# Performance work log

Measured on AMD Instinct MI355X. Metric: run time of the kernel, lower is better.

## Reference

```python
import jax, jax.numpy as jnp
import numpy as np
from jax import lax

T, B, I, H = 512, 256, 128, 256

def setup_inputs() -> dict:
    key = jax.random.key(0)
    k1, k2, k3, k4 = jax.random.split(key, 4)
    x = jax.random.normal(k1, (T, B, I), dtype=jnp.float32)
    h0 = jnp.zeros((B, H), dtype=jnp.float32)
    Wi = jax.random.normal(k2, (H, I), dtype=jnp.float32) * (1.0 / np.sqrt(I))
    Wh = jax.random.normal(k3, (H, H), dtype=jnp.float32) * (1.0 / np.sqrt(H))
    bh = jax.random.normal(k4, (H,), dtype=jnp.float32) * 0.01
    return {"x": x, "h0": h0, "Wi": Wi, "Wh": Wh, "bh": bh}

def reference(x, h0, Wi, Wh, bh):
    # Precompute input projection for all timesteps: [T, B, H]
    xi = jnp.einsum("tbi,hi->tbh", x, Wi) + bh
    def step(h, xi_t):
        h_new = jnp.tanh(xi_t + h @ Wh.T)
        return h_new, h_new
    _, hs = lax.scan(step, h0, xi)
    return hs  # [T, B, H] hidden states, matching torch stack(out[1:])
```

## Files before the change

### kernel.cpp

```cpp
#include <hip/hip_runtime.h>
#include <hip/hip_bf16.h>
#include <math.h>

#define TT 512
#define BB 256
#define II 128
#define HH 256

#define TANH_S 2.885390043258667f


#define FCHUNK(CNT, A0,A1,B0,B1,C0,C1,D0,D1, H0,H1) \
        "s_waitcnt lgkmcnt(" CNT ")\n" \
        "v_pk_fma_f32 v[32:33], v[" A0 "], v[" H0 "], v[32:33]\n" \
        "v_pk_fma_f32 v[34:35], v[" B0 "], v[" H0 "], v[34:35]\n" \
        "v_pk_fma_f32 v[36:37], v[" C0 "], v[" H0 "], v[36:37]\n" \
        "v_pk_fma_f32 v[38:39], v[" D0 "], v[" H0 "], v[38:39]\n" \
        "v_pk_fma_f32 v[32:33], v[" A1 "], v[" H1 "], v[32:33]\n" \
        "v_pk_fma_f32 v[34:35], v[" B1 "], v[" H1 "], v[34:35]\n" \
        "v_pk_fma_f32 v[36:37], v[" C1 "], v[" H1 "], v[36:37]\n" \
        "v_pk_fma_f32 v[38:39], v[" D1 "], v[" H1 "], v[38:39]\n"

#define SCALE_PAIR(P) "v_pk_mul_f32 v[" P "], v[" P "], v[26:27]\n"

__global__ __launch_bounds__(512, 2) void rnn_fused_kernel(
    const float* __restrict__ x,  const float* __restrict__ h0,
    const float* __restrict__ Wi, const float* __restrict__ Wh,
    const float* __restrict__ bh, float* __restrict__ out)
{
    __shared__ float hbuf[928];

    const int tid  = threadIdx.x;
    const int b    = blockIdx.x;
    const int lane = tid & 63;
    const int q    = tid >> 6;
    const int kg   = (lane & 3) | ((lane >> 1) & 4);
    const int cg   = ((lane >> 2) & 1) | ((lane >> 3) & 6);
    const int col0 = 32 * q + 4 * cg;
    const int col  = col0 + (kg & 3);

    const float* wp  = Wh + (size_t)col0 * HH + kg * 32;
    const float* wip = Wi + (size_t)col0 * II + kg * 16;
    const float* iob = out + (size_t)b * HH;
    const float* xb  = x   + (size_t)b * II;
    unsigned hbase = (unsigned)(size_t)&hbuf[0];
    unsigned hvr = hbase + kg * 208;
    unsigned hvw = hbase + 0x800 + q * 208 + (4 * cg + (kg & 3)) * 4;
    unsigned vxw = hbase + 0x800 + (tid >> 2) * 208 + 128 + 16 * (tid & 3);
    unsigned vxo = (unsigned)(16 * tid) + 0x20000u;
    unsigned vxomax = (unsigned)(16 * tid) + 511u * 0x20000u;
    unsigned vho = (unsigned)(col * 4);
    float bhv = bh[col] * TANH_S;
    unsigned long long m0   = __ballot((lane & 1) != 0);
    unsigned long long m1   = __ballot((lane & 2) != 0);
    unsigned long long msk  = __ballot(kg < 4);
    unsigned long long mskx = __ballot(tid < 32);

    if (tid < HH) hbuf[(tid >> 5) * 52 + (tid & 31)] = h0[(size_t)b * HH + tid];
    if (tid < II) hbuf[(tid >> 4) * 52 + 32 + (tid & 15)] = xb[tid];
    __syncthreads();

    asm volatile(
        "global_load_dwordx4 v[64:67],   %[wp], off\n"
        "global_load_dwordx4 v[68:71],   %[wp], off offset:16\n"
        "global_load_dwordx4 v[72:75],   %[wp], off offset:32\n"
        "global_load_dwordx4 v[76:79],   %[wp], off offset:48\n"
        "global_load_dwordx4 v[80:83],   %[wp], off offset:64\n"
        "global_load_dwordx4 v[84:87],   %[wp], off offset:80\n"
        "global_load_dwordx4 v[88:91],   %[wp], off offset:96\n"
        "global_load_dwordx4 v[92:95],   %[wp], off offset:112\n"
        "global_load_dwordx4 v[96:99],   %[wp], off offset:1024\n"
        "global_load_dwordx4 v[100:103], %[wp], off offset:1040\n"
        "global_load_dwordx4 v[104:107], %[wp], off offset:1056\n"
        "global_load_dwordx4 v[108:111], %[wp], off offset:1072\n"
        "global_load_dwordx4 v[112:115], %[wp], off offset:1088\n"
        "global_load_dwordx4 v[116:119], %[wp], off offset:1104\n"
        "global_load_dwordx4 v[120:123], %[wp], off offset:1120\n"
        "global_load_dwordx4 v[124:127], %[wp], off offset:1136\n"
        "global_load_dwordx4 v[128:131], %[wp], off offset:2048\n"
        "global_load_dwordx4 v[132:135], %[wp], off offset:2064\n"
        "global_load_dwordx4 v[136:139], %[wp], off offset:2080\n"
        "global_load_dwordx4 v[140:143], %[wp], off offset:2096\n"
        "global_load_dwordx4 v[144:147], %[wp], off offset:2112\n"
        "global_load_dwordx4 v[148:151], %[wp], off offset:2128\n"
        "global_load_dwordx4 v[152:155], %[wp], off offset:2144\n"
        "global_load_dwordx4 v[156:159], %[wp], off offset:2160\n"
        "global_load_dwordx4 v[160:163], %[wp], off offset:3072\n"
        "global_load_dwordx4 v[164:167], %[wp], off offset:3088\n"
        "global_load_dwordx4 v[168:171], %[wp], off offset:3104\n"
        "global_load_dwordx4 v[172:175], %[wp], off offset:3120\n"
        "global_load_dwordx4 v[176:179], %[wp], off offset:3136\n"
        "global_load_dwordx4 v[180:183], %[wp], off offset:3152\n"
        "global_load_dwordx4 v[184:187], %[wp], off offset:3168\n"
        "global_load_dwordx4 v[188:191], %[wp], off offset:3184\n"
        "global_load_dwordx4 v[192:195], %[wip], off\n"
        "global_load_dwordx4 v[196:199], %[wip], off offset:16\n"
        "global_load_dwordx4 v[200:203], %[wip], off offset:32\n"
        "global_load_dwordx4 v[204:207], %[wip], off offset:48\n"
        "global_load_dwordx4 v[208:211], %[wip], off offset:512\n"
        "global_load_dwordx4 v[212:215], %[wip], off offset:528\n"
        "global_load_dwordx4 v[216:219], %[wip], off offset:544\n"
        "global_load_dwordx4 v[220:223], %[wip], off offset:560\n"
        "global_load_dwordx4 v[224:227], %[wip], off offset:1024\n"
        "global_load_dwordx4 v[228:231], %[wip], off offset:1040\n"
        "global_load_dwordx4 v[232:235], %[wip], off offset:1056\n"
        "global_load_dwordx4 v[236:239], %[wip], off offset:1072\n"
        "global_load_dwordx4 v[240:243], %[wip], off offset:1536\n"
        "global_load_dwordx4 v[244:247], %[wip], off offset:1552\n"
        "global_load_dwordx4 v[248:251], %[wip], off offset:1568\n"
        "global_load_dwordx4 v[252:255], %[wip], off offset:1584\n"
        "v_mov_b32 v16, %[hvr]\n"
        "v_mov_b32 v17, %[hvw]\n"
        "v_mov_b32 v18, %[vxo]\n"
        "v_mov_b32 v19, %[bhv]\n"
        "v_mov_b32 v24, %[vxw]\n"
        "v_mov_b32 v25, %[vho]\n"
        "s_movk_i32 s82, 0x200\n"
        "s_waitcnt vmcnt(0)\n"
        "v_mov_b32 v26, 0x4038aa3b\n"
        "v_mov_b32 v27, 0x4038aa3b\n"
        SCALE_PAIR("64:65")   SCALE_PAIR("66:67")   SCALE_PAIR("68:69")   SCALE_PAIR("70:71")
        SCALE_PAIR("72:73")   SCALE_PAIR("74:75")   SCALE_PAIR("76:77")   SCALE_PAIR("78:79")
        SCALE_PAIR("80:81")   SCALE_PAIR("82:83")   SCALE_PAIR("84:85")   SCALE_PAIR("86:87")
        SCALE_PAIR("88:89")   SCALE_PAIR("90:91")   SCALE_PAIR("92:93")   SCALE_PAIR("94:95")
        SCALE_PAIR("96:97")   SCALE_PAIR("98:99")   SCALE_PAIR("100:101") SCALE_PAIR("102:103")
        SCALE_PAIR("104:105") SCALE_PAIR("106:107") SCALE_PAIR("108:109") SCALE_PAIR("110:111")
        SCALE_PAIR("112:113") SCALE_PAIR("114:115") SCALE_PAIR("116:117") SCALE_PAIR("118:119")
        SCALE_PAIR("120:121") SCALE_PAIR("122:123") SCALE_PAIR("124:125") SCALE_PAIR("126:127")
        SCALE_PAIR("128:129") SCALE_PAIR("130:131") SCALE_PAIR("132:133") SCALE_PAIR("134:135")
        SCALE_PAIR("136:137") SCALE_PAIR("138:139") SCALE_PAIR("140:141") SCALE_PAIR("142:143")
        SCALE_PAIR("144:145") SCALE_PAIR("146:147") SCALE_PAIR("148:149") SCALE_PAIR("150:151")
        SCALE_PAIR("152:153") SCALE_PAIR("154:155") SCALE_PAIR("156:157") SCALE_PAIR("158:159")
        SCALE_PAIR("160:161") SCALE_PAIR("162:163") SCALE_PAIR("164:165") SCALE_PAIR("166:167")
        SCALE_PAIR("168:169") SCALE_PAIR("170:171") SCALE_PAIR("172:173") SCALE_PAIR("174:175")
        SCALE_PAIR("176:177") SCALE_PAIR("178:179") SCALE_PAIR("180:181") SCALE_PAIR("182:183")
        SCALE_PAIR("184:185") SCALE_PAIR("186:187") SCALE_PAIR("188:189") SCALE_PAIR("190:191")
        SCALE_PAIR("192:193") SCALE_PAIR("194:195") SCALE_PAIR("196:197") SCALE_PAIR("198:199")
        SCALE_PAIR("200:201") SCALE_PAIR("202:203") SCALE_PAIR("204:205") SCALE_PAIR("206:207")
        SCALE_PAIR("208:209") SCALE_PAIR("210:211") SCALE_PAIR("212:213") SCALE_PAIR("214:215")
        SCALE_PAIR("216:217") SCALE_PAIR("218:219") SCALE_PAIR("220:221") SCALE_PAIR("222:223")
        SCALE_PAIR("224:225") SCALE_PAIR("226:227") SCALE_PAIR("228:229") SCALE_PAIR("230:231")
        SCALE_PAIR("232:233") SCALE_PAIR("234:235") SCALE_PAIR("236:237") SCALE_PAIR("238:239")
        SCALE_PAIR("240:241") SCALE_PAIR("242:243") SCALE_PAIR("244:245") SCALE_PAIR("246:247")
        SCALE_PAIR("248:249") SCALE_PAIR("250:251") SCALE_PAIR("252:253") SCALE_PAIR("254:255")
        "LTOP_%=:\n"
        "s_and_saveexec_b64 s[86:87], %[mskx]\n"
        "global_load_dwordx4 v[20:23], v18, %[xb]\n"
        "s_mov_b64 exec, s[86:87]\n"
        "v_add_u32 v18, 0x20000, v18\n"
        "v_min_u32 v18, %[vxomax], v18\n"
        "ds_read_b128 v[40:43], v16\n"
        "ds_read_b128 v[44:47], v16 offset:16\n"
        "ds_read_b128 v[48:51], v16 offset:32\n"
        "ds_read_b128 v[52:55], v16 offset:48\n"
        "ds_read_b128 v[56:59], v16 offset:64\n"
        "ds_read_b128 v[60:63], v16 offset:80\n"
        "s_waitcnt lgkmcnt(5)\n"
        "v_pk_mul_f32 v[32:33], v[64:65],   v[40:41]\n"
        "v_pk_mul_f32 v[34:35], v[96:97],   v[40:41]\n"
        "v_pk_mul_f32 v[36:37], v[128:129], v[40:41]\n"
        "v_pk_mul_f32 v[38:39], v[160:161], v[40:41]\n"
        "v_pk_fma_f32 v[32:33], v[66:67],   v[42:43], v[32:33]\n"
        "v_pk_fma_f32 v[34:35], v[98:99],   v[42:43], v[34:35]\n"
        "v_pk_fma_f32 v[36:37], v[130:131], v[42:43], v[36:37]\n"
        "v_pk_fma_f32 v[38:39], v[162:163], v[42:43], v[38:39]\n"
        "ds_read_b128 v[40:43], v16 offset:96\n"
        FCHUNK("5","68:69","70:71","100:101","102:103","132:133","134:135","164:165","166:167","44:45","46:47")
        "ds_read_b128 v[44:47], v16 offset:112\n"
        FCHUNK("5","72:73","74:75","104:105","106:107","136:137","138:139","168:169","170:171","48:49","50:51")
        "ds_read_b128 v[48:51], v16 offset:128\n"
        FCHUNK("5","76:77","78:79","108:109","110:111","140:141","142:143","172:173","174:175","52:53","54:55")
        "ds_read_b128 v[52:55], v16 offset:144\n"
        FCHUNK("5","80:81","82:83","112:113","114:115","144:145","146:147","176:177","178:179","56:57","58:59")
        "ds_read_b128 v[56:59], v16 offset:160\n"
        FCHUNK("5","84:85","86:87","116:117","118:119","148:149","150:151","180:181","182:183","60:61","62:63")
        "ds_read_b128 v[60:63], v16 offset:176\n"
        FCHUNK("5","88:89","90:91","120:121","122:123","152:153","154:155","184:185","186:187","40:41","42:43")
        FCHUNK("4","92:93","94:95","124:125","126:127","156:157","158:159","188:189","190:191","44:45","46:47")
        FCHUNK("3","192:193","194:195","208:209","210:211","224:225","226:227","240:241","242:243","48:49","50:51")
        FCHUNK("2","196:197","198:199","212:213","214:215","228:229","230:231","244:245","246:247","52:53","54:55")
        FCHUNK("1","200:201","202:203","216:217","218:219","232:233","234:235","248:249","250:251","56:57","58:59")
        FCHUNK("0","204:205","206:207","220:221","222:223","236:237","238:239","252:253","254:255","60:61","62:63")
        "v_add_f32 v26, v32, v33\n"
        "v_add_f32 v27, v34, v35\n"
        "v_add_f32 v28, v36, v37\n"
        "v_add_f32 v29, v38, v39\n"
        "v_add_f32 v26, v26, v26 quad_perm:[1,0,3,2] row_mask:0xf bank_mask:0xf\n"
        "v_add_f32 v27, v27, v27 quad_perm:[1,0,3,2] row_mask:0xf bank_mask:0xf\n"
        "v_add_f32 v28, v28, v28 quad_perm:[1,0,3,2] row_mask:0xf bank_mask:0xf\n"
        "v_add_f32 v29, v29, v29 quad_perm:[1,0,3,2] row_mask:0xf bank_mask:0xf\n"
        "v_add_f32 v26, v26, v26 quad_perm:[2,3,0,1] row_mask:0xf bank_mask:0xf\n"
        "v_add_f32 v27, v27, v27 quad_perm:[2,3,0,1] row_mask:0xf bank_mask:0xf\n"
        "v_add_f32 v28, v28, v28 quad_perm:[2,3,0,1] row_mask:0xf bank_mask:0xf\n"
        "v_add_f32 v29, v29, v29 quad_perm:[2,3,0,1] row_mask:0xf bank_mask:0xf\n"
        "v_add_f32 v26, v26, v26 row_ror:8 row_mask:0xf bank_mask:0xf\n"
        "v_add_f32 v27, v27, v27 row_ror:8 row_mask:0xf bank_mask:0xf\n"
        "v_add_f32 v28, v28, v28 row_ror:8 row_mask:0xf bank_mask:0xf\n"
        "v_add_f32 v29, v29, v29 row_ror:8 row_mask:0xf bank_mask:0xf\n"
        "v_cndmask_b32 v30, v26, v27, %[m0]\n"
        "v_cndmask_b32 v31, v28, v29, %[m0]\n"
        "v_cndmask_b32 v30, v30, v31, %[m1]\n"
        "v_add_f32 v30, v30, v19\n"
        "v_exp_f32 v31, v30\n"
        "s_nop 0\n"
        "v_add_f32 v31, 1.0, v31\n"
        "v_rcp_f32 v31, v31\n"
        "s_nop 0\n"
        "v_fma_f32 v30, -2.0, v31, 1.0\n"
        "s_and_saveexec_b64 s[84:85], %[msk]\n"
        "ds_write_b32 v17, v30\n"
        "s_mov_b64 exec, s[84:85]\n"
        "v_xor_b32 v17, 0x800, v17\n"
        "global_store_dword v25, v30, %[iob]\n"
        "v_add_u32 v25, 0x40000, v25\n"
        "s_waitcnt vmcnt(1)\n"
        "s_and_saveexec_b64 s[86:87], %[mskx]\n"
        "ds_write_b128 v24, v[20:23]\n"
        "s_mov_b64 exec, s[86:87]\n"
        "v_xor_b32 v24, 0x800, v24\n"
        "s_waitcnt lgkmcnt(0)\n"
        "s_barrier\n"
        "v_xor_b32 v16, 0x800, v16\n"
        "s_sub_u32 s82, s82, 1\n"
        "s_cmp_lg_u32 s82, 0\n"
        "s_cbranch_scc1 LTOP_%=\n"
        :
        : [wp] "v"(wp), [wip] "v"(wip), [iob] "s"(iob), [xb] "s"(xb),
          [hvr] "v"(hvr), [hvw] "v"(hvw), [vxo] "v"(vxo),
          [vxomax] "v"(vxomax), [vxw] "v"(vxw), [vho] "v"(vho),
          [bhv] "v"(bhv),
          [m0] "s"(m0), [m1] "s"(m1), [msk] "s"(msk), [mskx] "s"(mskx)
        : "memory", "scc", "s82", "s84", "s85", "s86", "s87",
          "v16","v17","v18","v19","v20","v21","v22","v23",
          "v24","v25","v26","v27","v28","v29","v30","v31",
          "v32","v33","v34","v35","v36","v37","v38","v39",
          "v40","v41","v42","v43","v44","v45","v46","v47",
          "v48","v49","v50","v51","v52","v53","v54","v55",
          "v56","v57","v58","v59","v60","v61","v62","v63",
          "v64","v65","v66","v67","v68","v69","v70","v71",
          "v72","v73","v74","v75","v76","v77","v78","v79",
          "v80","v81","v82","v83","v84","v85","v86","v87",
          "v88","v89","v90","v91","v92","v93","v94","v95",
          "v96","v97","v98","v99","v100","v101","v102","v103",
          "v104","v105","v106","v107","v108","v109","v110","v111",
          "v112","v113","v114","v115","v116","v117","v118","v119",
          "v120","v121","v122","v123","v124","v125","v126","v127",
          "v128","v129","v130","v131","v132","v133","v134","v135",
          "v136","v137","v138","v139","v140","v141","v142","v143",
          "v144","v145","v146","v147","v148","v149","v150","v151",
          "v152","v153","v154","v155","v156","v157","v158","v159",
          "v160","v161","v162","v163","v164","v165","v166","v167",
          "v168","v169","v170","v171","v172","v173","v174","v175",
          "v176","v177","v178","v179","v180","v181","v182","v183",
          "v184","v185","v186","v187","v188","v189","v190","v191",
          "v192","v193","v194","v195","v196","v197","v198","v199",
          "v200","v201","v202","v203","v204","v205","v206","v207",
          "v208","v209","v210","v211","v212","v213","v214","v215",
          "v216","v217","v218","v219","v220","v221","v222","v223",
          "v224","v225","v226","v227","v228","v229","v230","v231",
          "v232","v233","v234","v235","v236","v237","v238","v239",
          "v240","v241","v242","v243","v244","v245","v246","v247",
          "v248","v249","v250","v251","v252","v253","v254","v255");
}

extern "C" void kernel_launch(void* const* d_in, const int* in_sizes, int n_in,
                              void* d_out, int out_size, void* d_ws, size_t ws_size,
                              hipStream_t stream) {
    const float* x  = (const float*)d_in[0];
    const float* h0 = (const float*)d_in[1];
    const float* Wi = (const float*)d_in[2];
    const float* Wh = (const float*)d_in[3];
    const float* bh = (const float*)d_in[4];
    float* out = (float*)d_out;

    rnn_fused_kernel<<<BB, 512, 0, stream>>>(x, h0, Wi, Wh, bh, out);
}
```

Baseline: 343.4 us.

## Prefetch x two steps ahead with double-buffered registers and unroll loop by two

The x-tile global load now runs two timesteps ahead, using two alternating register sets (v[20:23] and v[26:29]) instead of one step ahead. The loop body is unrolled by two, with two peeled prologue iterations. The x write to LDS moves before the reduction so the vmcnt wait sits further from the load. This aims to hide global load latency on the serial recurrence critical path. It costs more code size, and the reduction temporaries are moved to v32-v38 to free v26-v29.

```diff
diff --git a/kernel.cpp b/kernel.cpp
--- a/kernel.cpp
+++ b/kernel.cpp
@@ -20,6 +20,95 @@
         "v_pk_fma_f32 v[34:35], v[" B1 "], v[" H1 "], v[34:35]\n" \
         "v_pk_fma_f32 v[36:37], v[" C1 "], v[" H1 "], v[36:37]\n" \
         "v_pk_fma_f32 v[38:39], v[" D1 "], v[" H1 "], v[38:39]\n"
+
+#define FBODY(XNR, XCR, VC) \
+         \
+        "s_and_saveexec_b64 s[86:87], %[mskx]\n" \
+        "global_load_dwordx4 " XNR ", v18, %[xb]\n" \
+        "s_mov_b64 exec, s[86:87]\n" \
+        "v_add_u32 v18, 0x20000, v18\n" \
+        "v_min_u32 v18, %[vxomax], v18\n" \
+         \
+        "ds_read_b128 v[40:43], v16\n" \
+        "ds_read_b128 v[44:47], v16 offset:16\n" \
+        "ds_read_b128 v[48:51], v16 offset:32\n" \
+        "ds_read_b128 v[52:55], v16 offset:48\n" \
+        "ds_read_b128 v[56:59], v16 offset:64\n" \
+        "ds_read_b128 v[60:63], v16 offset:80\n" \
+         \
+        "s_waitcnt lgkmcnt(5)\n" \
+        "v_pk_mul_f32 v[32:33], v[64:65],   v[40:41]\n" \
+        "v_pk_mul_f32 v[34:35], v[96:97],   v[40:41]\n" \
+        "v_pk_mul_f32 v[36:37], v[128:129], v[40:41]\n" \
+        "v_pk_mul_f32 v[38:39], v[160:161], v[40:41]\n" \
+        "v_pk_fma_f32 v[32:33], v[66:67],   v[42:43], v[32:33]\n" \
+        "v_pk_fma_f32 v[34:35], v[98:99],   v[42:43], v[34:35]\n" \
+        "v_pk_fma_f32 v[36:37], v[130:131], v[42:43], v[36:37]\n" \
+        "v_pk_fma_f32 v[38:39], v[162:163], v[42:43], v[38:39]\n" \
+        "ds_read_b128 v[40:43], v16 offset:96\n" \
+        FCHUNK("5","68:69","70:71","100:101","102:103","132:133","134:135","164:165","166:167","44:45","46:47") \
+        "ds_read_b128 v[44:47], v16 offset:112\n" \
+        FCHUNK("5","72:73","74:75","104:105","106:107","136:137","138:139","168:169","170:171","48:49","50:51") \
+        "ds_read_b128 v[48:51], v16 offset:128\n" \
+        FCHUNK("5","76:77","78:79","108:109","110:111","140:141","142:143","172:173","174:175","52:53","54:55") \
+        "ds_read_b128 v[52:55], v16 offset:144\n" \
+        FCHUNK("5","80:81","82:83","112:113","114:115","144:145","146:147","176:177","178:179","56:57","58:59") \
+        "ds_read_b128 v[56:59], v16 offset:160\n" \
+        FCHUNK("5","84:85","86:87","116:117","118:119","148:149","150:151","180:181","182:183","60:61","62:63") \
+        "ds_read_b128 v[60:63], v16 offset:176\n" \
+        FCHUNK("5","88:89","90:91","120:121","122:123","152:153","154:155","184:185","186:187","40:41","42:43") \
+        FCHUNK("4","92:93","94:95","124:125","126:127","156:157","158:159","188:189","190:191","44:45","46:47") \
+        FCHUNK("3","192:193","194:195","208:209","210:211","224:225","226:227","240:241","242:243","48:49","50:51") \
+        FCHUNK("2","196:197","198:199","212:213","214:215","228:229","230:231","244:245","246:247","52:53","54:55") \
+        FCHUNK("1","200:201","202:203","216:217","218:219","232:233","234:235","248:249","250:251","56:57","58:59") \
+        FCHUNK("0","204:205","206:207","220:221","222:223","236:237","238:239","252:253","254:255","60:61","62:63") \
+         \
+        "s_waitcnt vmcnt(" VC ")\n" \
+        "s_and_saveexec_b64 s[86:87], %[mskx]\n" \
+        "ds_write_b128 v24, " XCR "\n" \
+        "s_mov_b64 exec, s[86:87]\n" \
+        "v_xor_b32 v24, 0x800, v24\n" \
+         \
+        "v_add_f32 v32, v32, v33\n" \
+        "v_add_f32 v34, v34, v35\n" \
+        "v_add_f32 v36, v36, v37\n" \
+        "v_add_f32 v38, v38, v39\n" \
+         \
+        "v_add_f32 v32, v32, v32 quad_perm:[1,0,3,2] row_mask:0xf bank_mask:0xf\n" \
+        "v_add_f32 v34, v34, v34 quad_perm:[1,0,3,2] row_mask:0xf bank_mask:0xf\n" \
+        "v_add_f32 v36, v36, v36 quad_perm:[1,0,3,2] row_mask:0xf bank_mask:0xf\n" \
+        "v_add_f32 v38, v38, v38 quad_perm:[1,0,3,2] row_mask:0xf bank_mask:0xf\n" \
+        "v_add_f32 v32, v32, v32 quad_perm:[2,3,0,1] row_mask:0xf bank_mask:0xf\n" \
+        "v_add_f32 v34, v34, v34 quad_perm:[2,3,0,1] row_mask:0xf bank_mask:0xf\n" \
+        "v_add_f32 v36, v36, v36 quad_perm:[2,3,0,1] row_mask:0xf bank_mask:0xf\n" \
+        "v_add_f32 v38, v38, v38 quad_perm:[2,3,0,1] row_mask:0xf bank_mask:0xf\n" \
+        "v_add_f32 v32, v32, v32 row_ror:8 row_mask:0xf bank_mask:0xf\n" \
+        "v_add_f32 v34, v34, v34 row_ror:8 row_mask:0xf bank_mask:0xf\n" \
+        "v_add_f32 v36, v36, v36 row_ror:8 row_mask:0xf bank_mask:0xf\n" \
+        "v_add_f32 v38, v38, v38 row_ror:8 row_mask:0xf bank_mask:0xf\n" \
+         \
+        "v_cndmask_b32 v30, v32, v34, %[m0]\n" \
+        "v_cndmask_b32 v31, v36, v38, %[m0]\n" \
+        "v_cndmask_b32 v30, v30, v31, %[m1]\n" \
+         \
+        "v_add_f32 v30, v30, v19\n" \
+        "v_exp_f32 v31, v30\n" \
+        "s_nop 0\n" \
+        "v_add_f32 v31, 1.0, v31\n" \
+        "v_rcp_f32 v31, v31\n" \
+        "s_nop 0\n" \
+        "v_fma_f32 v30, -2.0, v31, 1.0\n" \
+         \
+        "s_and_saveexec_b64 s[84:85], %[msk]\n" \
+        "ds_write_b32 v17, v30\n" \
+        "s_mov_b64 exec, s[84:85]\n" \
+        "v_xor_b32 v17, 0x800, v17\n" \
+         \
+        "global_store_dword v25, v30, %[iob]\n" \
+        "v_add_u32 v25, 0x40000, v25\n" \
+        "s_waitcnt lgkmcnt(0)\n" \
+        "s_barrier\n" \
+        "v_xor_b32 v16, 0x800, v16\n"
 
 #define SCALE_PAIR(P) "v_pk_mul_f32 v[" P "], v[" P "], v[26:27]\n"
 
@@ -115,7 +204,6 @@
         "v_mov_b32 v19, %[bhv]\n"
         "v_mov_b32 v24, %[vxw]\n"
         "v_mov_b32 v25, %[vho]\n"
-        "s_movk_i32 s82, 0x200\n"
         "s_waitcnt vmcnt(0)\n"
         "v_mov_b32 v26, 0x4038aa3b\n"
         "v_mov_b32 v27, 0x4038aa3b\n"
@@ -143,84 +231,16 @@
         SCALE_PAIR("232:233") SCALE_PAIR("234:235") SCALE_PAIR("236:237") SCALE_PAIR("238:239")
         SCALE_PAIR("240:241") SCALE_PAIR("242:243") SCALE_PAIR("244:245") SCALE_PAIR("246:247")
         SCALE_PAIR("248:249") SCALE_PAIR("250:251") SCALE_PAIR("252:253") SCALE_PAIR("254:255")
-        "LTOP_%=:\n"
         "s_and_saveexec_b64 s[86:87], %[mskx]\n"
-        "global_load_dwordx4 v[20:23], v18, %[xb]\n"
+        "global_load_dwordx4 v[26:29], v18, %[xb]\n"
         "s_mov_b64 exec, s[86:87]\n"
         "v_add_u32 v18, 0x20000, v18\n"
-        "v_min_u32 v18, %[vxomax], v18\n"
-        "ds_read_b128 v[40:43], v16\n"
-        "ds_read_b128 v[44:47], v16 offset:16\n"
-        "ds_read_b128 v[48:51], v16 offset:32\n"
-        "ds_read_b128 v[52:55], v16 offset:48\n"
-        "ds_read_b128 v[56:59], v16 offset:64\n"
-        "ds_read_b128 v[60:63], v16 offset:80\n"
-        "s_waitcnt lgkmcnt(5)\n"
-        "v_pk_mul_f32 v[32:33], v[64:65],   v[40:41]\n"
-        "v_pk_mul_f32 v[34:35], v[96:97],   v[40:41]\n"
-        "v_pk_mul_f32 v[36:37], v[128:129], v[40:41]\n"
-        "v_pk_mul_f32 v[38:39], v[160:161], v[40:41]\n"
-        "v_pk_fma_f32 v[32:33], v[66:67],   v[42:43], v[32:33]\n"
-        "v_pk_fma_f32 v[34:35], v[98:99],   v[42:43], v[34:35]\n"
-        "v_pk_fma_f32 v[36:37], v[130:131], v[42:43], v[36:37]\n"
-        "v_pk_fma_f32 v[38:39], v[162:163], v[42:43], v[38:39]\n"
-        "ds_read_b128 v[40:43], v16 offset:96\n"
-        FCHUNK("5","68:69","70:71","100:101","102:103","132:133","134:135","164:165","166:167","44:45","46:47")
-        "ds_read_b128 v[44:47], v16 offset:112\n"
-        FCHUNK("5","72:73","74:75","104:105","106:107","136:137","138:139","168:169","170:171","48:49","50:51")
-        "ds_read_b128 v[48:51], v16 offset:128\n"
-        FCHUNK("5","76:77","78:79","108:109","110:111","140:141","142:143","172:173","174:175","52:53","54:55")
-        "ds_read_b128 v[52:55], v16 offset:144\n"
-        FCHUNK("5","80:81","82:83","112:113","114:115","144:145","146:147","176:177","178:179","56:57","58:59")
-        "ds_read_b128 v[56:59], v16 offset:160\n"
-        FCHUNK("5","84:85","86:87","116:117","118:119","148:149","150:151","180:181","182:183","60:61","62:63")
-        "ds_read_b128 v[60:63], v16 offset:176\n"
-        FCHUNK("5","88:89","90:91","120:121","122:123","152:153","154:155","184:185","186:187","40:41","42:43")
-        FCHUNK("4","92:93","94:95","124:125","126:127","156:157","158:159","188:189","190:191","44:45","46:47")
-        FCHUNK("3","192:193","194:195","208:209","210:211","224:225","226:227","240:241","242:243","48:49","50:51")
-        FCHUNK("2","196:197","198:199","212:213","214:215","228:229","230:231","244:245","246:247","52:53","54:55")
-        FCHUNK("1","200:201","202:203","216:217","218:219","232:233","234:235","248:249","250:251","56:57","58:59")
-        FCHUNK("0","204:205","206:207","220:221","222:223","236:237","238:239","252:253","254:255","60:61","62:63")
-        "v_add_f32 v26, v32, v33\n"
-        "v_add_f32 v27, v34, v35\n"
-        "v_add_f32 v28, v36, v37\n"
-        "v_add_f32 v29, v38, v39\n"
-        "v_add_f32 v26, v26, v26 quad_perm:[1,0,3,2] row_mask:0xf bank_mask:0xf\n"
-        "v_add_f32 v27, v27, v27 quad_perm:[1,0,3,2] row_mask:0xf bank_mask:0xf\n"
-        "v_add_f32 v28, v28, v28 quad_perm:[1,0,3,2] row_mask:0xf bank_mask:0xf\n"
-        "v_add_f32 v29, v29, v29 quad_perm:[1,0,3,2] row_mask:0xf bank_mask:0xf\n"
-        "v_add_f32 v26, v26, v26 quad_perm:[2,3,0,1] row_mask:0xf bank_mask:0xf\n"
-        "v_add_f32 v27, v27, v27 quad_perm:[2,3,0,1] row_mask:0xf bank_mask:0xf\n"
-        "v_add_f32 v28, v28, v28 quad_perm:[2,3,0,1] row_mask:0xf bank_mask:0xf\n"
-        "v_add_f32 v29, v29, v29 quad_perm:[2,3,0,1] row_mask:0xf bank_mask:0xf\n"
-        "v_add_f32 v26, v26, v26 row_ror:8 row_mask:0xf bank_mask:0xf\n"
-        "v_add_f32 v27, v27, v27 row_ror:8 row_mask:0xf bank_mask:0xf\n"
-        "v_add_f32 v28, v28, v28 row_ror:8 row_mask:0xf bank_mask:0xf\n"
-        "v_add_f32 v29, v29, v29 row_ror:8 row_mask:0xf bank_mask:0xf\n"
-        "v_cndmask_b32 v30, v26, v27, %[m0]\n"
-        "v_cndmask_b32 v31, v28, v29, %[m0]\n"
-        "v_cndmask_b32 v30, v30, v31, %[m1]\n"
-        "v_add_f32 v30, v30, v19\n"
-        "v_exp_f32 v31, v30\n"
-        "s_nop 0\n"
-        "v_add_f32 v31, 1.0, v31\n"
-        "v_rcp_f32 v31, v31\n"
-        "s_nop 0\n"
-        "v_fma_f32 v30, -2.0, v31, 1.0\n"
-        "s_and_saveexec_b64 s[84:85], %[msk]\n"
-        "ds_write_b32 v17, v30\n"
-        "s_mov_b64 exec, s[84:85]\n"
-        "v_xor_b32 v17, 0x800, v17\n"
-        "global_store_dword v25, v30, %[iob]\n"
-        "v_add_u32 v25, 0x40000, v25\n"
-        "s_waitcnt vmcnt(1)\n"
-        "s_and_saveexec_b64 s[86:87], %[mskx]\n"
-        "ds_write_b128 v24, v[20:23]\n"
-        "s_mov_b64 exec, s[86:87]\n"
-        "v_xor_b32 v24, 0x800, v24\n"
-        "s_waitcnt lgkmcnt(0)\n"
-        "s_barrier\n"
-        "v_xor_b32 v16, 0x800, v16\n"
+        "s_movk_i32 s82, 0xFF\n"
+        FBODY("v[20:23]", "v[26:29]", "0")
+        FBODY("v[26:29]", "v[20:23]", "2")
+        "LTOP_%=:\n"
+        FBODY("v[20:23]", "v[26:29]", "2")
+        FBODY("v[26:29]", "v[20:23]", "2")
         "s_sub_u32 s82, s82, 1\n"
         "s_cmp_lg_u32 s82, 0\n"
         "s_cbranch_scc1 LTOP_%=\n"
```

Measured after the change: 337.4 us. No clear change (-1.7%).
